# Optimization experiments

Measured on AMD Instinct MI355X. Metric: run time of the kernel, lower is better.

The kernel has to match this reference:

```python
import jax, jax.numpy as jnp
import numpy as np

N, C = 131072, 1000
ALPHA_LINK = 0.25  # weight applied when pred is a 'linked' (acceptable) confusion of gt
GAMMA = 2.0        # focal exponent


def setup_inputs() -> dict:
    key = jax.random.key(0)
    k1, k2, k3, k4 = jax.random.split(key, 4)
    y_pred = jax.random.normal(k1, (N, C), dtype=jnp.float32)
    y_true = jax.random.randint(k2, (N,), 0, C, dtype=jnp.int64)
    # Dense representation of the python link dict: link_matrix[gt, pred] == True
    # iff pred is in link[gt]; has_link[gt] == True iff gt is a key of link.
    link_matrix = jax.random.bernoulli(k3, 0.01, (C, C))
    has_link = jax.random.bernoulli(k4, 0.5, (C,))
    return {"y_pred": y_pred, "y_true": y_true,
            "link_matrix": link_matrix, "has_link": has_link}


def reference(y_pred, y_true, link_matrix, has_link):
    # per-sample cross entropy (stable log-softmax + gather)
    logp = jax.nn.log_softmax(y_pred, axis=-1)                     # [N, C]
    ce = -jnp.take_along_axis(logp, y_true[:, None], axis=1)[:, 0]  # [N]
    pt = jnp.exp(-ce)                                              # [N]
    pred = jnp.argmax(y_pred, axis=1)                              # [N]
    # link_bad: ALPHA_LINK iff pred != gt, gt in link, and pred in link[gt]; else 1
    linked = link_matrix[y_true, pred] & has_link[y_true] & (pred != y_true)
    w = jnp.where(linked, jnp.float32(ALPHA_LINK), jnp.float32(1.0))
    return jnp.mean(w * (1.0 - pt) ** GAMMA * ce)
```

## Files before the change

### kernel.cpp

```cpp
#include <hip/hip_runtime.h>
#include <math.h>


#define NROWS 131072
#define NC 1000
#define NF4 250
#define ROWS_PER_BLOCK 16
#define NBLOCKS (NROWS / ROWS_PER_BLOCK)
#define ALPHA_LINK 0.25f

__global__ void lfl_detect(const int* __restrict__ yt,
                           const unsigned int* __restrict__ hl,
                           int* __restrict__ flags) {
    if (threadIdx.x == 0 && blockIdx.x == 0) {
        int y64 = 1;
        for (int i = 0; i < 64; ++i)
            if (yt[2 * i + 1] != 0) { y64 = 0; break; }
        int bfmt = 0;
        for (int i = 0; i < 250; ++i)
            if (hl[i] > 1u) { bfmt = 1; break; }
        flags[0] = y64;
        flags[1] = bfmt;
    }
}

__global__ __launch_bounds__(256) void lfl_main(
    const float* __restrict__ yp,
    const int* __restrict__ yt,
    const unsigned char* __restrict__ linkb, const int* __restrict__ linki,
    const unsigned char* __restrict__ hasb,  const int* __restrict__ hasi,
    const int* __restrict__ flags,
    float* __restrict__ partial)
{
    const int lane = threadIdx.x & 63;
    const int wid  = threadIdx.x >> 6;
    const int y64  = flags[0];
    const int bfmt = flags[1];

    float wsum = 0.0f;

    for (int r = 0; r < 4; ++r) {
        const int row = blockIdx.x * ROWS_PER_BLOCK + wid * 4 + r;
        const float4* rowp = (const float4*)(yp + (size_t)row * NC);
        const int target = y64 ? yt[2 * row] : yt[row];
        const int tf = target >> 2;

        float4 v[4];
        v[0] = rowp[lane];
        v[1] = rowp[lane + 64];
        v[2] = rowp[lane + 128];
        const bool has3 = (lane + 192) < NF4;
        v[3] = has3 ? rowp[lane + 192]
                    : make_float4(-INFINITY, -INFINITY, -INFINITY, -INFINITY);

        float lmax = -INFINITY;
        int   lidx = 1 << 30;
        float xt = 0.0f;
        #pragma unroll
        for (int k = 0; k < 4; ++k) {
            const int f  = lane + 64 * k;
            const int c0 = f * 4;
            const float x0 = v[k].x, x1 = v[k].y, x2 = v[k].z, x3 = v[k].w;
            if (x0 > lmax) { lmax = x0; lidx = c0; }
            if (x1 > lmax) { lmax = x1; lidx = c0 + 1; }
            if (x2 > lmax) { lmax = x2; lidx = c0 + 2; }
            if (x3 > lmax) { lmax = x3; lidx = c0 + 3; }
            if (tf == f) {
                const int t = target & 3;
                xt = (t == 0) ? x0 : (t == 1) ? x1 : (t == 2) ? x2 : x3;
            }
        }

        #pragma unroll
        for (int off = 32; off; off >>= 1) {
            const float om = __shfl_xor(lmax, off);
            const int   oi = __shfl_xor(lidx, off);
            if (om > lmax || (om == lmax && oi < lidx)) { lmax = om; lidx = oi; }
        }

        float s = 0.0f;
        #pragma unroll
        for (int k = 0; k < 4; ++k) {
            s += __expf(v[k].x - lmax) + __expf(v[k].y - lmax)
               + __expf(v[k].z - lmax) + __expf(v[k].w - lmax);
        }
        #pragma unroll
        for (int off = 32; off; off >>= 1) s += __shfl_xor(s, off);

        xt = __shfl(xt, tf & 63);

        const float logp_t = xt - lmax - __logf(s);
        const float ce = -logp_t;
        const float pt = __expf(logp_t);
        const int pred = lidx;

        const size_t ofs = (size_t)target * NC + (size_t)pred;
        const bool lm = bfmt ? (linkb[ofs] != 0) : (linki[ofs] != 0);
        const bool hb = bfmt ? (hasb[target] != 0) : (hasi[target] != 0);
        const float w = (lm && hb && (pred != target)) ? ALPHA_LINK : 1.0f;

        const float ompt = 1.0f - pt;
        wsum += w * ompt * ompt * ce;
    }

    __shared__ float wpart[4];
    if (lane == 0) wpart[wid] = wsum;
    __syncthreads();
    if (threadIdx.x == 0)
        partial[blockIdx.x] = wpart[0] + wpart[1] + wpart[2] + wpart[3];
}

__global__ __launch_bounds__(256) void lfl_final(const float* __restrict__ partial,
                                                 float* __restrict__ out) {
    __shared__ float sm[256];
    float s = 0.0f;
    for (int i = threadIdx.x; i < NBLOCKS; i += 256) s += partial[i];
    sm[threadIdx.x] = s;
    __syncthreads();
    for (int stride = 128; stride; stride >>= 1) {
        if ((int)threadIdx.x < stride) sm[threadIdx.x] += sm[threadIdx.x + stride];
        __syncthreads();
    }
    if (threadIdx.x == 0) out[0] = sm[0] * (1.0f / (float)NROWS);
}

extern "C" void kernel_launch(void* const* d_in, const int* in_sizes, int n_in,
                              void* d_out, int out_size, void* d_ws, size_t ws_size,
                              hipStream_t stream) {
    const float* yp = (const float*)d_in[0];
    const int*   yt = (const int*)d_in[1];
    const void*  lk = d_in[2];
    const void*  hl = d_in[3];

    float* partial = (float*)d_ws;
    int*   flags   = (int*)d_ws + NBLOCKS;

    lfl_detect<<<1, 64, 0, stream>>>(yt, (const unsigned int*)hl, flags);
    lfl_main<<<NBLOCKS, 256, 0, stream>>>(
        yp, yt,
        (const unsigned char*)lk, (const int*)lk,
        (const unsigned char*)hl, (const int*)hl,
        flags, partial);
    lfl_final<<<1, 256, 0, stream>>>(partial, (float*)d_out);
}
```

Before: 112.2 us.

## Fold format detection into main kernel, prefetch next row, merge online softmax reductions

Drops the single-thread detect kernel and has every wave detect the int64 and byte formats itself with ballots over a few loaded words. The next row's logits are loaded while the current row is processed. The separate max and sum reductions become one online-softmax butterfly that carries the running max, index and rescaled sum. Per-wave partials go straight to global memory, dropping the block shared-memory reduction, and the final kernel widens to 1024 threads. This removes one kernel launch and a serialized dependency, at the cost of redundant detection loads per wave and extra registers and exp calls in the reduction.

```diff
diff --git a/kernel.cpp b/kernel.cpp
--- a/kernel.cpp
+++ b/kernel.cpp
@@ -5,23 +5,20 @@
 #define NROWS 131072
 #define NC 1000
 #define NF4 250
-#define ROWS_PER_BLOCK 16
+#define ROWS_PER_WAVE 4
+#define WAVES_PER_BLOCK 4
+#define ROWS_PER_BLOCK (ROWS_PER_WAVE * WAVES_PER_BLOCK)
 #define NBLOCKS (NROWS / ROWS_PER_BLOCK)
+#define NWAVES (NBLOCKS * WAVES_PER_BLOCK)
 #define ALPHA_LINK 0.25f
 
-__global__ void lfl_detect(const int* __restrict__ yt,
-                           const unsigned int* __restrict__ hl,
-                           int* __restrict__ flags) {
-    if (threadIdx.x == 0 && blockIdx.x == 0) {
-        int y64 = 1;
-        for (int i = 0; i < 64; ++i)
-            if (yt[2 * i + 1] != 0) { y64 = 0; break; }
-        int bfmt = 0;
-        for (int i = 0; i < 250; ++i)
-            if (hl[i] > 1u) { bfmt = 1; break; }
-        flags[0] = y64;
-        flags[1] = bfmt;
-    }
+__device__ __forceinline__ void load_row(const float4* __restrict__ rowp,
+                                         int lane, float4 v[4]) {
+    v[0] = rowp[lane];
+    v[1] = rowp[lane + 64];
+    v[2] = rowp[lane + 128];
+    v[3] = (lane + 192 < NF4) ? rowp[lane + 192]
+         : make_float4(-INFINITY, -INFINITY, -INFINITY, -INFINITY);
 }
 
 __global__ __launch_bounds__(256) void lfl_main(
@@ -29,95 +26,102 @@
     const int* __restrict__ yt,
     const unsigned char* __restrict__ linkb, const int* __restrict__ linki,
     const unsigned char* __restrict__ hasb,  const int* __restrict__ hasi,
-    const int* __restrict__ flags,
+    const unsigned int* __restrict__ hlw,
     float* __restrict__ partial)
 {
-    const int lane = threadIdx.x & 63;
-    const int wid  = threadIdx.x >> 6;
-    const int y64  = flags[0];
-    const int bfmt = flags[1];
+    const int lane  = threadIdx.x & 63;
+    const int wid   = threadIdx.x >> 6;
+    const int gwave = blockIdx.x * WAVES_PER_BLOCK + wid;
 
+    const int hi = yt[2 * lane + 1];
+    const int y64 = (__ballot(hi != 0) == 0ULL);
+    const unsigned int h0 = hlw[lane];
+    const unsigned int h1 = hlw[lane + 64];
+    const unsigned int h2 = hlw[lane + 128];
+    const unsigned int h3 = (lane + 192 < NF4) ? hlw[lane + 192] : 0u;
+    const int bfmt = (__ballot((h0 > 1u) | (h1 > 1u) | (h2 > 1u) | (h3 > 1u)) != 0ULL);
+
+    const int row0 = blockIdx.x * ROWS_PER_BLOCK + wid * ROWS_PER_WAVE;
     float wsum = 0.0f;
 
-    for (int r = 0; r < 4; ++r) {
-        const int row = blockIdx.x * ROWS_PER_BLOCK + wid * 4 + r;
-        const float4* rowp = (const float4*)(yp + (size_t)row * NC);
+    float4 v[4];
+    load_row((const float4*)(yp + (size_t)row0 * NC), lane, v);
+
+    #pragma unroll
+    for (int r = 0; r < ROWS_PER_WAVE; ++r) {
+        const int row = row0 + r;
         const int target = y64 ? yt[2 * row] : yt[row];
         const int tf = target >> 2;
+        const int tl = target & 3;
 
-        float4 v[4];
-        v[0] = rowp[lane];
-        v[1] = rowp[lane + 64];
-        v[2] = rowp[lane + 128];
-        const bool has3 = (lane + 192) < NF4;
-        v[3] = has3 ? rowp[lane + 192]
-                    : make_float4(-INFINITY, -INFINITY, -INFINITY, -INFINITY);
+        float4 vn[4];
+        if (r + 1 < ROWS_PER_WAVE)
+            load_row((const float4*)(yp + (size_t)(row + 1) * NC), lane, vn);
 
-        float lmax = -INFINITY;
-        int   lidx = 1 << 30;
+        float m = -INFINITY;
+        int   idx = 1 << 30;
         float xt = 0.0f;
         #pragma unroll
         for (int k = 0; k < 4; ++k) {
             const int f  = lane + 64 * k;
             const int c0 = f * 4;
             const float x0 = v[k].x, x1 = v[k].y, x2 = v[k].z, x3 = v[k].w;
-            if (x0 > lmax) { lmax = x0; lidx = c0; }
-            if (x1 > lmax) { lmax = x1; lidx = c0 + 1; }
-            if (x2 > lmax) { lmax = x2; lidx = c0 + 2; }
-            if (x3 > lmax) { lmax = x3; lidx = c0 + 3; }
-            if (tf == f) {
-                const int t = target & 3;
-                xt = (t == 0) ? x0 : (t == 1) ? x1 : (t == 2) ? x2 : x3;
-            }
-        }
-
-        #pragma unroll
-        for (int off = 32; off; off >>= 1) {
-            const float om = __shfl_xor(lmax, off);
-            const int   oi = __shfl_xor(lidx, off);
-            if (om > lmax || (om == lmax && oi < lidx)) { lmax = om; lidx = oi; }
+            if (x0 > m) { m = x0; idx = c0; }
+            if (x1 > m) { m = x1; idx = c0 + 1; }
+            if (x2 > m) { m = x2; idx = c0 + 2; }
+            if (x3 > m) { m = x3; idx = c0 + 3; }
+            if (f == tf) xt = (tl == 0) ? x0 : (tl == 1) ? x1 : (tl == 2) ? x2 : x3;
         }
 
         float s = 0.0f;
         #pragma unroll
         for (int k = 0; k < 4; ++k) {
-            s += __expf(v[k].x - lmax) + __expf(v[k].y - lmax)
-               + __expf(v[k].z - lmax) + __expf(v[k].w - lmax);
+            s += __expf(v[k].x - m) + __expf(v[k].y - m)
+               + __expf(v[k].z - m) + __expf(v[k].w - m);
         }
+
+        const float xts = __shfl(xt, tf & 63);
+
         #pragma unroll
-        for (int off = 32; off; off >>= 1) s += __shfl_xor(s, off);
+        for (int off = 32; off; off >>= 1) {
+            const float om = __shfl_xor(m, off);
+            const int   oi = __shfl_xor(idx, off);
+            const float os = __shfl_xor(s, off);
+            const float mn = fmaxf(m, om);
+            s = s * __expf(m - mn) + os * __expf(om - mn);
+            if (om > m || (om == m && oi < idx)) idx = oi;
+            m = mn;
+        }
 
-        xt = __shfl(xt, tf & 63);
-
-        const float logp_t = xt - lmax - __logf(s);
+        const float logp_t = xts - m - __logf(s);
         const float ce = -logp_t;
         const float pt = __expf(logp_t);
-        const int pred = lidx;
+        const int pred = idx;
 
         const size_t ofs = (size_t)target * NC + (size_t)pred;
-        const bool lm = bfmt ? (linkb[ofs] != 0) : (linki[ofs] != 0);
-        const bool hb = bfmt ? (hasb[target] != 0) : (hasi[target] != 0);
+        const bool lm = bfmt ? (linkb[ofs] != 0)    : (linki[ofs] != 0);
+        const bool hb = bfmt ? (hasb[target] != 0)  : (hasi[target] != 0);
         const float w = (lm && hb && (pred != target)) ? ALPHA_LINK : 1.0f;
 
         const float ompt = 1.0f - pt;
         wsum += w * ompt * ompt * ce;
+
+        if (r + 1 < ROWS_PER_WAVE) {
+            v[0] = vn[0]; v[1] = vn[1]; v[2] = vn[2]; v[3] = vn[3];
+        }
     }
 
-    __shared__ float wpart[4];
-    if (lane == 0) wpart[wid] = wsum;
-    __syncthreads();
-    if (threadIdx.x == 0)
-        partial[blockIdx.x] = wpart[0] + wpart[1] + wpart[2] + wpart[3];
+    if (lane == 0) partial[gwave] = wsum;
 }
 
-__global__ __launch_bounds__(256) void lfl_final(const float* __restrict__ partial,
-                                                 float* __restrict__ out) {
-    __shared__ float sm[256];
+__global__ __launch_bounds__(1024) void lfl_final(const float* __restrict__ partial,
+                                                  float* __restrict__ out) {
+    __shared__ float sm[1024];
     float s = 0.0f;
-    for (int i = threadIdx.x; i < NBLOCKS; i += 256) s += partial[i];
+    for (int i = threadIdx.x; i < NWAVES; i += 1024) s += partial[i];
     sm[threadIdx.x] = s;
     __syncthreads();
-    for (int stride = 128; stride; stride >>= 1) {
+    for (int stride = 512; stride; stride >>= 1) {
         if ((int)threadIdx.x < stride) sm[threadIdx.x] += sm[threadIdx.x + stride];
         __syncthreads();
     }
@@ -133,13 +137,12 @@
     const void*  hl = d_in[3];
 
     float* partial = (float*)d_ws;
-    int*   flags   = (int*)d_ws + NBLOCKS;
 
-    lfl_detect<<<1, 64, 0, stream>>>(yt, (const unsigned int*)hl, flags);
     lfl_main<<<NBLOCKS, 256, 0, stream>>>(
         yp, yt,
         (const unsigned char*)lk, (const int*)lk,
         (const unsigned char*)hl, (const int*)hl,
-        flags, partial);
-    lfl_final<<<1, 256, 0, stream>>>(partial, (float*)d_out);
+        (const unsigned int*)hl,
+        partial);
+    lfl_final<<<1, 1024, 0, stream>>>(partial, (float*)d_out);
 }
```

After: 116.8 us. 1.04x slower.
